# Performance work log

Hardware: AMD Instinct MI355X
Metric: run time of the kernel (lower is better)

## Reference

```python
import jax, jax.numpy as jnp
import numpy as np

B, P, C = 32, 8732, 21
TOP_K = 200
CONF_THRESH = 0.01
NMS_THRESH = 0.45
VAR0, VAR1 = 0.1, 0.2  # VOC PRIOR_BOX VARIANCE


def setup_inputs() -> dict:
    key = jax.random.key(0)
    k1, k2, k3 = jax.random.split(key, 3)
    loc_data = jax.random.normal(k1, (B, P, 4), jnp.float32)
    conf_data = jax.random.uniform(k2, (B, P, C), jnp.float32)
    prior_data = jax.random.uniform(k3, (P, 4), jnp.float32)
    return {"loc_data": loc_data, "conf_data": conf_data, "prior_data": prior_data}


def _decode(loc, priors):
    # priors are (cx, cy, w, h); returns (x1, y1, x2, y2)
    cxcy = priors[:, :2] + loc[:, :2] * VAR0 * priors[:, 2:]
    wh = priors[:, 2:] * jnp.exp(loc[:, 2:] * VAR1)
    x1y1 = cxcy - wh * 0.5
    return jnp.concatenate([x1y1, x1y1 + wh], axis=1)  # [P,4]


def _nms_class(boxes, scores):
    # boxes [P,4], scores [P] -> [TOP_K,5] rows of (score, x1, y1, x2, y2)
    s = jnp.where(scores > CONF_THRESH, scores, -1.0)
    top_s, idx = jax.lax.top_k(s, TOP_K)          # descending scores
    b = boxes[idx]                                 # [K,4]
    valid = top_s > CONF_THRESH
    x1, y1, x2, y2 = b[:, 0], b[:, 1], b[:, 2], b[:, 3]
    area = (x2 - x1) * (y2 - y1)
    # pairwise intersection / IoU [K,K]
    xx1 = jnp.maximum(x1[:, None], x1[None, :])
    yy1 = jnp.maximum(y1[:, None], y1[None, :])
    xx2 = jnp.minimum(x2[:, None], x2[None, :])
    yy2 = jnp.minimum(y2[:, None], y2[None, :])
    inter = jnp.clip(xx2 - xx1, 0.0) * jnp.clip(yy2 - yy1, 0.0)
    union = area[:, None] + area[None, :] - inter
    iou = inter / union
    ar = jnp.arange(TOP_K)

    def step(carry, j):
        kept, suppressed = carry
        is_kept = valid[j] & ~suppressed[j]
        kept = kept.at[j].set(is_kept)
        suppressed = suppressed | (is_kept & (iou[j] > NMS_THRESH) & (ar > j))
        return (kept, suppressed), None

    (kept, _), _ = jax.lax.scan(
        step, (jnp.zeros(TOP_K, bool), jnp.zeros(TOP_K, bool)), ar)
    # compact kept rows to the front (matches output[i, cl, :count] = ...)
    pos = jnp.cumsum(kept) - 1
    safe = jnp.where(kept, pos, TOP_K)
    rows = jnp.concatenate([top_s[:, None], b], axis=1)  # [K,5]
    out = jnp.zeros((TOP_K + 1, 5), rows.dtype).at[safe].set(rows)[:TOP_K]
    return out


def reference(loc_data, conf_data, prior_data):
    def per_image(loc, conf):
        boxes = _decode(loc, prior_data)           # [P,4]
        return jax.vmap(lambda s: _nms_class(boxes, s), in_axes=1)(conf)  # [C,K,5]

    out = jax.vmap(per_image)(loc_data, conf_data)  # [B,C,K,5]
    return out.at[:, 0].set(0.0)  # class 0 (background) is skipped in original
```

## Files before the change

kernel.cpp:

```cpp
#include <hip/hip_runtime.h>
#include <stdint.h>

#define B_ 32
#define P_ 8732
#define C_ 21
#define TOPK 200
#define TGT 228
#define TGT0 300
#define SUBCAP 28
#define NCH2 35
#define NSLOT (NCH2 * SUBCAP)
#define CONF_T 0.01f
#define NMS_T 0.45f
#define NT 512
#define KV4 5
#define NTASK (B_ * C_)

__device__ __forceinline__ uint32_t f2s(float f) {
    uint32_t u = __float_as_uint(f);
    return (u & 0x80000000u) ? ~u : (u | 0x80000000u);
}
__device__ __forceinline__ float s2f(uint32_t s) {
    uint32_t b = (s & 0x80000000u) ? (s & 0x7FFFFFFFu) : ~s;
    return __uint_as_float(b);
}
__device__ __forceinline__ uint32_t keyof(float v) {
    return f2s((v > CONF_T) ? v : -1.0f);
}
__device__ __forceinline__ uint32_t thr0() {
    return f2s(1.0f - (float)TGT0 / (float)P_);
}

__global__ __launch_bounds__(256) void scatter_cands(const float* __restrict__ conf,
                                                     uint32_t* __restrict__ gccnt,
                                                     uint64_t* __restrict__ gcand) {
    const int b = blockIdx.x / NCH2;
    const int ch = blockIdx.x % NCH2;
    const int p0 = ch * 256;
    const int n = min(256, P_ - p0);
    const int tid = threadIdx.x;
    const int lane = tid & 63;
    const int cs = tid >> 6;
    __shared__ float tile[256 * C_];
    const float4* src4 = (const float4*)(conf + ((size_t)b * P_ + p0) * C_);
    float4* tile4 = (float4*)tile;
    const int tot4 = (n * C_) >> 2;
    for (int i = tid; i < tot4; i += 256) tile4[i] = src4[i];
    __syncthreads();
    const uint32_t T0 = thr0();
    for (int c = (cs == 0 ? 4 : cs); c < C_; c += 4) {
        uint32_t kk[4];
        #pragma unroll
        for (int k = 0; k < 4; ++k) {
            const int r = lane + 64 * k;
            if (r < n) kk[k] = keyof(tile[r * C_ + c]);
            else       kk[k] = 0u;
        }
        const unsigned long long m0 = __ballot(kk[0] >= T0);
        const unsigned long long m1 = __ballot(kk[1] >= T0);
        const unsigned long long m2 = __ballot(kk[2] >= T0);
        const unsigned long long m3 = __ballot(kk[3] >= T0);
        const int c0 = __popcll(m0), c1 = __popcll(m1), c2 = __popcll(m2), c3 = __popcll(m3);
        const int total = c0 + c1 + c2 + c3;
        const int task = b * C_ + c;
        uint64_t* dst = gcand + ((size_t)task * NCH2 + ch) * SUBCAP;
        {
            const unsigned long long below = (1ull << lane) - 1ull;
            const int cum[4] = {0, c0, c0 + c1, c0 + c1 + c2};
            const unsigned long long mm[4] = {m0, m1, m2, m3};
            #pragma unroll
            for (int k = 0; k < 4; ++k) {
                if (kk[k] >= T0) {
                    const int pos = cum[k] + __popcll(mm[k] & below);
                    if (pos < SUBCAP) {
                        const int p = p0 + lane + 64 * k;
                        dst[pos] = ((uint64_t)kk[k] << 32) | (uint32_t)(~(uint32_t)p);
                    }
                }
            }
        }
        if (lane == 0) gccnt[(size_t)task * NCH2 + ch] = (uint32_t)total;
    }
}

template<bool HASWS>
__global__ __launch_bounds__(NT, 6) void detect_kernel(
    const float* __restrict__ loc, const float* __restrict__ prior,
    const uint32_t* __restrict__ gccnt, const uint64_t* __restrict__ gcand,
    const float* __restrict__ conf, float* __restrict__ out)
{
    const int task = blockIdx.x;
    const int b = task / C_;
    const int c = task % C_;
    const int tid = threadIdx.x;
    const int lane = tid & 63;
    float* outp = out + (size_t)task * TOPK * 5;

    if (c == 0) {
        for (int e = tid; e < TOPK * 5; e += NT) outp[e] = 0.0f;
        return;
    }

    __shared__ uint64_t cand[256];
    __shared__ float4 bbox[TOPK];
    __shared__ float bs[TOPK];
    __shared__ float sar[TOPK];
    __shared__ unsigned long long msk[TOPK * 4];
    __shared__ unsigned long long vmask[4];
    __shared__ int order[TOPK];
    __shared__ int s_cnt, s_nk;
    __shared__ int s_c2[2];
    __shared__ int s_c3[3];
    __shared__ uint32_t s_ccnt[NCH2];
    __shared__ int s_gc, s_bad;

    const uint32_t T0 = thr0();

    if (tid == 0) s_cnt = 0;
    if (tid < 2) s_c2[tid] = 0;
    if (tid < 3) s_c3[tid] = 0;
    if (HASWS && tid < NCH2) s_ccnt[tid] = gccnt[(size_t)task * NCH2 + tid];
    __syncthreads();
    if (HASWS && tid < 64) {
        uint32_t cc = (lane < NCH2) ? s_ccnt[lane] : 0u;
        int bad = (cc > SUBCAP) ? 1 : 0;
        int tot = (int)cc;
        #pragma unroll
        for (int d = 1; d < 64; d <<= 1) {
            tot += __shfl_down(tot, d);
            bad |= __shfl_down(bad, d);
        }
        if (lane == 0) { s_gc = tot; s_bad = bad; }
    }
    __syncthreads();

    const bool fast = HASWS && !s_bad && s_gc >= TOPK;
    const int gc = HASWS ? s_gc : 0;

    uint64_t vc0 = 0, vc1 = 0;
    bool val0 = false, val1 = false;
    uint4 kv[KV4];
    if (fast) {
        const uint64_t* gp = gcand + (size_t)task * NSLOT;
        {
            const int ch0 = tid / SUBCAP, i0 = tid - ch0 * SUBCAP;
            if (i0 < (int)s_ccnt[ch0]) { vc0 = gp[tid]; val0 = true; }
        }
        const int s1 = tid + NT;
        if (s1 < NSLOT) {
            const int ch1 = s1 / SUBCAP, i1 = s1 - ch1 * SUBCAP;
            if (i1 < (int)s_ccnt[ch1]) { vc1 = gp[s1]; val1 = true; }
        }
    } else {
        const float* sp = conf + (size_t)b * P_ * C_ + c;
        #pragma unroll
        for (int r = 0; r < KV4; ++r) {
            uint32_t uu[4];
            #pragma unroll
            for (int c4 = 0; c4 < 4; ++c4) {
                int p = (tid + r * NT) * 4 + c4;
                if (p < P_) {
                    float v = sp[(size_t)p * C_];
                    v = (v > CONF_T) ? v : -1.0f;
                    uu[c4] = f2s(v);
                } else uu[c4] = 0u;
            }
            kv[r] = make_uint4(uu[0], uu[1], uu[2], uu[3]);
        }
    }

    if (fast) {
        const uint32_t k0 = (uint32_t)(vc0 >> 32);
        const uint32_t k1 = (uint32_t)(vc1 >> 32);
        uint32_t vthr = T0;
        if (gc > 256) {
            uint32_t lo = T0, hi = 0xFFFFFFFFu;
            uint32_t t;
            {
                const float sc = s2f(T0);
                const float sn = 1.0f - (1.0f - sc) * (float)TGT / (float)gc;
                t = f2s(sn);
                if (!(t > lo && t < hi)) t = lo + ((hi - lo) >> 1);
            }
            for (int it = 0; ; ++it) {
                const int slot = it % 3;
                int my = (val0 && k0 >= t) + (val1 && k1 >= t);
                #pragma unroll
                for (int d = 1; d < 64; d <<= 1) my += __shfl_down(my, d);
                if (lane == 0) atomicAdd(&s_c3[slot], my);
                if (tid == 0) s_c3[(it + 1) % 3] = 0;
                __syncthreads();
                const int cnt = s_c3[slot];
                if (cnt >= TOPK && cnt <= 256) { vthr = t; break; }
                if (cnt > 256) lo = t; else hi = t;
                if (hi - lo <= 1) { vthr = lo; break; }
                uint32_t tn = 0;
                bool bis = (it >= 8) || (cnt == 0);
                if (!bis) {
                    const float sc = s2f(t);
                    const float sn = 1.0f - (1.0f - sc) * (float)TGT / (float)cnt;
                    tn = f2s(sn);
                    if (!(tn > lo && tn < hi)) bis = true;
                }
                if (bis) tn = lo + ((hi - lo) >> 1);
                t = tn;
            }
        }
        const bool p0v = val0 && k0 >= vthr;
        const bool p1v = val1 && k1 >= vthr;
        const unsigned long long mm0 = __ballot(p0v);
        const unsigned long long mm1 = __ballot(p1v);
        const int wtot = __popcll(mm0) + __popcll(mm1);
        int base = 0;
        if (lane == 0 && wtot) base = atomicAdd(&s_cnt, wtot);
        base = __shfl(base, 0);
        const unsigned long long below = (1ull << lane) - 1ull;
        const int o0 = base + __popcll(mm0 & below);
        const int o1 = base + __popcll(mm0) + __popcll(mm1 & below);
        if (p0v && o0 < 256) cand[o0] = vc0;
        if (p1v && o1 < 256) cand[o1] = vc1;
    } else {
        uint32_t lo = 0u, hi = 0xFFFFFFFFu;
        uint32_t t = f2s(1.0f - (float)TGT / (float)P_);
        uint32_t vthr = 0u;
        for (int it = 0; ; ++it) {
            const int slot = it & 1;
            int my = 0;
            #pragma unroll
            for (int r = 0; r < KV4; ++r)
                my += (kv[r].x >= t) + (kv[r].y >= t) + (kv[r].z >= t) + (kv[r].w >= t);
            #pragma unroll
            for (int d = 1; d < 64; d <<= 1) my += __shfl_down(my, d);
            if (lane == 0) atomicAdd(&s_c2[slot], my);
            __syncthreads();
            const int cnt = s_c2[slot];
            __syncthreads();
            if (tid == 0) s_c2[slot] = 0;
            if (cnt >= TOPK && cnt <= 256) { vthr = t; break; }
            if (cnt > 256) lo = t; else hi = t;
            if (hi - lo <= 1) { vthr = lo; break; }
            uint32_t tn = 0;
            bool bis = (it >= 8) || (cnt == 0);
            if (!bis) {
                const float sc = s2f(t);
                const float sn = 1.0f - (1.0f - sc) * (float)TGT / (float)cnt;
                tn = f2s(sn);
                if (!(tn > lo && tn < hi)) bis = true;
            }
            if (bis) tn = lo + ((hi - lo) >> 1);
            t = tn;
        }
        #pragma unroll
        for (int r = 0; r < KV4; ++r) {
            const int pb = (tid + r * NT) * 4;
            uint32_t uu[4] = {kv[r].x, kv[r].y, kv[r].z, kv[r].w};
            #pragma unroll
            for (int c4 = 0; c4 < 4; ++c4) {
                uint32_t u = uu[c4];
                if (u >= vthr) {
                    int pos = atomicAdd(&s_cnt, 1);
                    if (pos < 256) cand[pos] = ((uint64_t)u << 32) | (uint32_t)(~(uint32_t)(pb + c4));
                }
            }
        }
    }
    __syncthreads();
    if (tid < 256 && tid >= s_cnt) cand[tid] = 0ull;
    __syncthreads();

    uint64_t v = (tid < 256) ? cand[tid] : 0ull;
    for (int kk = 2; kk <= 256; kk <<= 1) {
        for (int j = kk >> 1; j > 0; j >>= 1) {
            if (j >= 64) {
                __syncthreads();
                if (tid < 256) cand[tid] = v;
                __syncthreads();
                if (tid < 256) {
                    uint64_t pv = cand[tid ^ j];
                    bool keepmax = (((tid & j) == 0) == ((tid & kk) == 0));
                    v = keepmax ? (v > pv ? v : pv) : (v < pv ? v : pv);
                }
            } else if (tid < 256) {
                uint64_t pv = __shfl_xor(v, j);
                bool keepmax = (((tid & j) == 0) == ((tid & kk) == 0));
                v = keepmax ? (v > pv ? v : pv) : (v < pv ? v : pv);
            }
        }
    }

    float my_sc = -1.0f;
    if (tid < TOPK) {
        uint32_t su = (uint32_t)(v >> 32);
        int p = (int)(~(uint32_t)v);
        my_sc = s2f(su);
        const float4 l4 = *(const float4*)(loc + ((size_t)b * P_ + p) * 4);
        const float4 pr = *(const float4*)(prior + (size_t)p * 4);
        float cx = __fadd_rn(pr.x, __fmul_rn(__fmul_rn(l4.x, 0.1f), pr.z));
        float cy = __fadd_rn(pr.y, __fmul_rn(__fmul_rn(l4.y, 0.1f), pr.w));
        float ew = (float)exp((double)__fmul_rn(l4.z, 0.2f));
        float eh = (float)exp((double)__fmul_rn(l4.w, 0.2f));
        float w  = __fmul_rn(pr.z, ew);
        float h  = __fmul_rn(pr.w, eh);
        float x1 = __fsub_rn(cx, __fmul_rn(w, 0.5f));
        float y1 = __fsub_rn(cy, __fmul_rn(h, 0.5f));
        float x2 = __fadd_rn(x1, w);
        float y2 = __fadd_rn(y1, h);
        bs[tid] = my_sc;
        bbox[tid] = make_float4(x1, y1, x2, y2);
        sar[tid] = __fmul_rn(__fsub_rn(x2, x1), __fsub_rn(y2, y1));
    }
    {
        unsigned long long bm = __ballot(tid < TOPK && my_sc > CONF_T);
        if (lane == 0 && tid < 256) vmask[tid >> 6] = bm;
    }
    __syncthreads();

    {
        const int wv = tid >> 6;
        float4 biA[4];
        float  aiA[4];
        #pragma unroll
        for (int t = 0; t < 4; ++t) {
            const int i = (t << 6) | lane;
            if (i < TOPK) {
                biA[t] = bbox[i];
                aiA[t] = __fmul_rn(__fsub_rn(biA[t].z, biA[t].x),
                                   __fsub_rn(biA[t].w, biA[t].y));
            } else {
                biA[t] = make_float4(0.0f, 0.0f, 0.0f, 0.0f);
                aiA[t] = 0.0f;
            }
        }
        for (int r = 0; r < 25; ++r) {
            const int j = (r << 3) | wv;
            const float4 bj = bbox[j];
            const float  aj = sar[j];
            unsigned long long* mrow = &msk[j * 4];
            #pragma unroll
            for (int t = 0; t < 4; ++t) {
                unsigned long long word = 0ull;
                if (((t << 6) | 63) > j) {
                    const int i = (t << 6) | lane;
                    bool sup = false;
                    if (i > j && i < TOPK) {
                        const float4 bi = biA[t];
                        float xx1 = fmaxf(bj.x, bi.x);
                        float yy1 = fmaxf(bj.y, bi.y);
                        float xx2 = fminf(bj.z, bi.z);
                        float yy2 = fminf(bj.w, bi.w);
                        float dx = fmaxf(__fsub_rn(xx2, xx1), 0.0f);
                        float dy = fmaxf(__fsub_rn(yy2, yy1), 0.0f);
                        float inter = __fmul_rn(dx, dy);
                        if (inter > 0.0f) {
                            float uni = __fsub_rn(__fadd_rn(aj, aiA[t]), inter);
                            float t45 = __fmul_rn(NMS_T, uni);
                            float mar = __fmul_rn(t45, 1e-6f);
                            sup = inter > __fadd_rn(t45, mar);
                            if (!sup && !(inter < __fsub_rn(t45, mar)))
                                sup = (inter / uni > NMS_T);
                        }
                    }
                    word = __ballot(sup);
                }
                if (lane == 0) mrow[t] = word;
            }
        }
    }
    __syncthreads();

    if (tid < 64) {
        const int L = tid;
        auto or_reduce = [&](unsigned long long x) {
            #pragma unroll
            for (int d = 1; d < 64; d <<= 1) x |= __shfl_xor(x, d);
            return x;
        };
        unsigned long long s1 = 0, s2 = 0, s3 = 0;
        int nk = 0;
        #pragma unroll
        for (int w = 0; w < 4; ++w) {
            const int j = (w << 6) | L;
            unsigned long long r0 = 0, r1 = 0, r2 = 0, r3 = 0;
            if (j < TOPK) {
                const unsigned long long* mr = &msk[j * 4];
                r0 = mr[0]; r1 = mr[1]; r2 = mr[2]; r3 = mr[3];
            }
            const unsigned long long rself = (w == 0) ? r0 : (w == 1) ? r1
                                           : (w == 2) ? r2 : r3;
            unsigned long long sw = (w == 0) ? 0ull : (w == 1) ? s1
                                  : (w == 2) ? s2 : s3;
            unsigned long long alive = vmask[w] & ~sw;
            unsigned long long pm = 0;
            while (alive) {
                int jl = __ffsll(alive) - 1;
                if (L == 0) order[nk] = (w << 6) | jl;
                ++nk;
                sw |= __shfl(rself, jl);
                pm |= (1ull << jl);
                alive &= ~(sw | (1ull << jl));
            }
            if (pm) {
                const bool picked = (pm >> L) & 1ull;
                if (w == 0) {
                    s1 |= or_reduce(picked ? r1 : 0ull);
                    s2 |= or_reduce(picked ? r2 : 0ull);
                    s3 |= or_reduce(picked ? r3 : 0ull);
                } else if (w == 1) {
                    s2 |= or_reduce(picked ? r2 : 0ull);
                    s3 |= or_reduce(picked ? r3 : 0ull);
                } else if (w == 2) {
                    s3 |= or_reduce(picked ? r3 : 0ull);
                }
            }
        }
        if (L == 0) s_nk = nk;
    }
    __syncthreads();

    const int nk = s_nk;
    for (int e = tid; e < TOPK * 5; e += NT) {
        int r = e / 5;
        int f = e - r * 5;
        float val = 0.0f;
        if (r < nk) {
            int j = order[r];
            float4 bb = bbox[j];
            val = (f == 0) ? bs[j] : (f == 1) ? bb.x : (f == 2) ? bb.y
                : (f == 3) ? bb.z : bb.w;
        }
        outp[e] = val;
    }
}

extern "C" void kernel_launch(void* const* d_in, const int* in_sizes, int n_in,
                              void* d_out, int out_size, void* d_ws, size_t ws_size,
                              hipStream_t stream) {
    const float* loc   = (const float*)d_in[0];
    const float* conf  = (const float*)d_in[1];
    const float* prior = (const float*)d_in[2];
    float* out = (float*)d_out;

    const size_t cnt_bytes  = (size_t)NTASK * NCH2 * sizeof(uint32_t);
    const size_t cand_bytes = (size_t)NTASK * NSLOT * sizeof(uint64_t);
    if (ws_size >= cnt_bytes + cand_bytes) {
        uint32_t* gccnt = (uint32_t*)d_ws;
        uint64_t* gcand = (uint64_t*)((char*)d_ws + cnt_bytes);
        scatter_cands<<<B_ * NCH2, 256, 0, stream>>>(conf, gccnt, gcand);
        detect_kernel<true><<<NTASK, NT, 0, stream>>>(loc, prior, gccnt, gcand, conf, out);
    } else {
        detect_kernel<false><<<NTASK, NT, 0, stream>>>(loc, prior, nullptr, nullptr, conf, out);
    }
}
```

Before: 132.2 us.

## Compute IoU suppression rows lazily only for kept boxes in a single wave

```diff
diff --git a/kernel.cpp b/kernel.cpp
--- a/kernel.cpp
+++ b/kernel.cpp
@@ -104,8 +104,6 @@
     __shared__ uint64_t cand[256];
     __shared__ float4 bbox[TOPK];
     __shared__ float bs[TOPK];
-    __shared__ float sar[TOPK];
-    __shared__ unsigned long long msk[TOPK * 4];
     __shared__ unsigned long long vmask[4];
     __shared__ int order[TOPK];
     __shared__ int s_cnt, s_nk;
@@ -307,7 +305,6 @@
         float y2 = __fadd_rn(y1, h);
         bs[tid] = my_sc;
         bbox[tid] = make_float4(x1, y1, x2, y2);
-        sar[tid] = __fmul_rn(__fsub_rn(x2, x1), __fsub_rn(y2, y1));
     }
     {
         unsigned long long bm = __ballot(tid < TOPK && my_sc > CONF_T);
@@ -315,13 +312,13 @@
     }
     __syncthreads();
 
-    {
-        const int wv = tid >> 6;
+    if (tid < 64) {
+        const int L = tid;
         float4 biA[4];
         float  aiA[4];
         #pragma unroll
         for (int t = 0; t < 4; ++t) {
-            const int i = (t << 6) | lane;
+            const int i = (t << 6) | L;
             if (i < TOPK) {
                 biA[t] = bbox[i];
                 aiA[t] = __fmul_rn(__fsub_rn(biA[t].z, biA[t].x),
@@ -331,16 +328,23 @@
                 aiA[t] = 0.0f;
             }
         }
-        for (int r = 0; r < 25; ++r) {
-            const int j = (r << 3) | wv;
-            const float4 bj = bbox[j];
-            const float  aj = sar[j];
-            unsigned long long* mrow = &msk[j * 4];
-            #pragma unroll
-            for (int t = 0; t < 4; ++t) {
-                unsigned long long word = 0ull;
-                if (((t << 6) | 63) > j) {
-                    const int i = (t << 6) | lane;
+        unsigned long long S0 = 0, S1 = 0, S2 = 0, S3 = 0;
+        int nk = 0;
+        #pragma unroll
+        for (int w = 0; w < 4; ++w) {
+            unsigned long long alive = vmask[w]
+                & ~((w == 0) ? S0 : (w == 1) ? S1 : (w == 2) ? S2 : S3);
+            while (alive) {
+                const int jl = __ffsll(alive) - 1;
+                const int j = (w << 6) | jl;
+                if (L == 0) order[nk] = j;
+                ++nk;
+                const float4 bj = bbox[j];
+                const float  aj = __fmul_rn(__fsub_rn(bj.z, bj.x),
+                                            __fsub_rn(bj.w, bj.y));
+                #pragma unroll
+                for (int t = 0; t < 4; ++t) {
+                    const int i = (t << 6) | L;
                     bool sup = false;
                     if (i > j && i < TOPK) {
                         const float4 bi = biA[t];
@@ -360,57 +364,12 @@
                                 sup = (inter / uni > NMS_T);
                         }
                     }
-                    word = __ballot(sup);
+                    const unsigned long long row = __ballot(sup);
+                    if (t == 0) S0 |= row; else if (t == 1) S1 |= row;
+                    else if (t == 2) S2 |= row; else S3 |= row;
                 }
-                if (lane == 0) mrow[t] = word;
-            }
-        }
-    }
-    __syncthreads();
-
-    if (tid < 64) {
-        const int L = tid;
-        auto or_reduce = [&](unsigned long long x) {
-            #pragma unroll
-            for (int d = 1; d < 64; d <<= 1) x |= __shfl_xor(x, d);
-            return x;
-        };
-        unsigned long long s1 = 0, s2 = 0, s3 = 0;
-        int nk = 0;
-        #pragma unroll
-        for (int w = 0; w < 4; ++w) {
-            const int j = (w << 6) | L;
-            unsigned long long r0 = 0, r1 = 0, r2 = 0, r3 = 0;
-            if (j < TOPK) {
-                const unsigned long long* mr = &msk[j * 4];
-                r0 = mr[0]; r1 = mr[1]; r2 = mr[2]; r3 = mr[3];
-            }
-            const unsigned long long rself = (w == 0) ? r0 : (w == 1) ? r1
-                                           : (w == 2) ? r2 : r3;
-            unsigned long long sw = (w == 0) ? 0ull : (w == 1) ? s1
-                                  : (w == 2) ? s2 : s3;
-            unsigned long long alive = vmask[w] & ~sw;
-            unsigned long long pm = 0;
-            while (alive) {
-                int jl = __ffsll(alive) - 1;
-                if (L == 0) order[nk] = (w << 6) | jl;
-                ++nk;
-                sw |= __shfl(rself, jl);
-                pm |= (1ull << jl);
-                alive &= ~(sw | (1ull << jl));
-            }
-            if (pm) {
-                const bool picked = (pm >> L) & 1ull;
-                if (w == 0) {
-                    s1 |= or_reduce(picked ? r1 : 0ull);
-                    s2 |= or_reduce(picked ? r2 : 0ull);
-                    s3 |= or_reduce(picked ? r3 : 0ull);
-                } else if (w == 1) {
-                    s2 |= or_reduce(picked ? r2 : 0ull);
-                    s3 |= or_reduce(picked ? r3 : 0ull);
-                } else if (w == 2) {
-                    s3 |= or_reduce(picked ? r3 : 0ull);
-                }
+                alive &= ~(1ull << jl);
+                alive &= ~((w == 0) ? S0 : (w == 1) ? S1 : (w == 2) ? S2 : S3);
             }
         }
         if (L == 0) s_nk = nk;
```

New measurement: 151.6 us. 1.15x slower.
